# Kernel optimization log

Hardware: AMD Instinct MI355X
Metric: run time of the kernel (lower is better)

Reference implementation:

```python
import jax, jax.numpy as jnp
import numpy as np

IN_CHS = 512
RED_CHS = int(IN_CHS * 0.25)  # 128
NUM_ACTIONS = 2
BATCH = 131072


def setup_inputs() -> dict:
    key = jax.random.key(0)
    kx, k1, k2 = jax.random.split(key, 3)
    x = jax.random.normal(kx, (BATCH, IN_CHS), dtype=jnp.float32)
    # conv_reduce: Linear(in_chs, reduced_chs), conv_expand: Linear(reduced_chs, 2)
    W1 = jax.random.normal(k1, (IN_CHS, RED_CHS), dtype=jnp.float32) * 0.02
    b1 = jnp.zeros((RED_CHS,), dtype=jnp.float32)
    W2 = jax.random.normal(k2, (RED_CHS, NUM_ACTIONS), dtype=jnp.float32) * 0.02
    b2 = jnp.zeros((NUM_ACTIONS,), dtype=jnp.float32)
    return {"x": x, "W1": W1, "b1": b1, "W2": W2, "b2": b2}


def reference(x, W1, b1, W2, b2):
    # tiny 2-layer MLP head
    h = jax.nn.relu(x @ W1 + b1)                 # [B, 128]
    logits = h @ W2 + b2                         # [B, 2]
    logp = jax.nn.log_softmax(logits, axis=1)    # softmax(dim=1) in log space
    # per-row categorical sampling (np.random.choice(p=attn[id])) via Gumbel-max,
    # fused instead of a Python loop with host sync
    skey = jax.random.fold_in(jax.random.key(0), 12345)
    g = jax.random.gumbel(skey, logp.shape, dtype=logp.dtype)
    actions = jnp.argmax(logp + g, axis=1).astype(jnp.int32)  # [B]
    return actions
```

## Files before the change

### kernel.cpp

```cpp
#include <hip/hip_runtime.h>
#include <stdint.h>
#include <math.h>


#define BM 128
#define BK 32
#define LDK 40
#define IN_CHS 512
#define RED_CHS 128
#define BATCH 131072

typedef __attribute__((ext_vector_type(8))) short bf16x8;
typedef __attribute__((ext_vector_type(4))) float f32x4;

__host__ __device__ inline void tf2x32(uint32_t k0, uint32_t k1,
                                       uint32_t x0, uint32_t x1,
                                       uint32_t* o0, uint32_t* o1) {
  uint32_t ks2 = k0 ^ k1 ^ 0x1BD11BDAu;
  x0 += k0; x1 += k1;
#define TFR(r) { x0 += x1; x1 = (x1 << r) | (x1 >> (32 - r)); x1 ^= x0; }
  TFR(13) TFR(15) TFR(26) TFR(6)
  x0 += k1; x1 += ks2 + 1u;
  TFR(17) TFR(29) TFR(16) TFR(24)
  x0 += ks2; x1 += k0 + 2u;
  TFR(13) TFR(15) TFR(26) TFR(6)
  x0 += k0; x1 += k1 + 3u;
  TFR(17) TFR(29) TFR(16) TFR(24)
  x0 += k1; x1 += ks2 + 4u;
  TFR(13) TFR(15) TFR(26) TFR(6)
  x0 += ks2; x1 += k0 + 5u;
#undef TFR
  *o0 = x0; *o1 = x1;
}

__device__ __forceinline__ float gumbel_from_bits(uint32_t bits) {
  uint32_t fb = (bits >> 9) | 0x3f800000u;
  float u = __uint_as_float(fb) - 1.0f;
  if (u == 0.0f) u = 1.175494350822287508e-38f;
  float t = -(float)log((double)u);
  return -(float)log((double)t);
}

__device__ __forceinline__ unsigned short f2bf(float f) {
  uint32_t u = __float_as_uint(f);
  return (unsigned short)((u + 0x7fffu + ((u >> 16) & 1u)) >> 16);
}
__device__ __forceinline__ float bf2f(unsigned short h) {
  return __uint_as_float(((uint32_t)h) << 16);
}

__global__ __launch_bounds__(256) void rl_head_mfma(
    const float* __restrict__ x, const float* __restrict__ W1,
    const float* __restrict__ b1, const float* __restrict__ W2,
    const float* __restrict__ b2, int* __restrict__ out,
    uint32_t fk0, uint32_t fk1) {
  __shared__ __align__(16) char smem[4 * BM * LDK * 2];
  unsigned short* Ah = (unsigned short*)smem;
  unsigned short* Al = Ah + BM * LDK;
  unsigned short* Bh = Al + BM * LDK;
  float* red = (float*)smem;

  const int tid = threadIdx.x;
  const int lane = tid & 63;
  const int w = tid >> 6;
  const int ln = lane & 15;
  const int quad = lane >> 4;
  const int row0 = blockIdx.x * BM;

  const int ar = tid >> 3;
  const int ak = (tid & 7) * 4;
  const int bc = tid & 127;
  const int bk0 = (tid >> 7) * 16;

  f32x4 acc[2][8];
#pragma unroll
  for (int i = 0; i < 2; ++i)
#pragma unroll
    for (int j = 0; j < 8; ++j) acc[i][j] = (f32x4)(0.0f);

  for (int kb = 0; kb < IN_CHS; kb += BK) {
    float4 av[4];
#pragma unroll
    for (int q = 0; q < 4; ++q)
      av[q] = *(const float4*)(&x[(size_t)(row0 + q * 32 + ar) * IN_CHS + kb + ak]);
    float bv[16];
#pragma unroll
    for (int i = 0; i < 16; ++i)
      bv[i] = W1[(size_t)(kb + bk0 + i) * RED_CHS + bc];

#pragma unroll
    for (int q = 0; q < 4; ++q) {
      const int r = q * 32 + ar;
      float f[4] = {av[q].x, av[q].y, av[q].z, av[q].w};
      ushort4 h4, l4;
      unsigned short* hp = (unsigned short*)&h4;
      unsigned short* lp = (unsigned short*)&l4;
#pragma unroll
      for (int c = 0; c < 4; ++c) {
        unsigned short h = f2bf(f[c]);
        hp[c] = h;
        lp[c] = f2bf(f[c] - bf2f(h));
      }
      *(ushort4*)(&Ah[r * LDK + ak]) = h4;
      *(ushort4*)(&Al[r * LDK + ak]) = l4;
    }
    {
      ushort4 h4[4], l4[4];
#pragma unroll
      for (int g = 0; g < 4; ++g) {
        unsigned short* hp = (unsigned short*)&h4[g];
        unsigned short* lp = (unsigned short*)&l4[g];
#pragma unroll
        for (int c = 0; c < 4; ++c) {
          float f = bv[g * 4 + c];
          unsigned short h = f2bf(f);
          hp[c] = h;
          lp[c] = f2bf(f - bf2f(h));
        }
      }
#pragma unroll
      for (int g = 0; g < 4; ++g) {
        *(ushort4*)(&Bh[bc * LDK + bk0 + g * 4]) = h4[g];
        *(ushort4*)(&Bh[BM * LDK + bc * LDK + bk0 + g * 4]) = l4[g];
      }
    }
    __syncthreads();

    const unsigned short* ap = &Ah[(w * 32 + ln) * LDK + quad * 8];
    bf16x8 ah0 = *(const bf16x8*)ap;
    bf16x8 ah1 = *(const bf16x8*)(ap + 16 * LDK);
    bf16x8 al0 = *(const bf16x8*)(ap + BM * LDK);
    bf16x8 al1 = *(const bf16x8*)(ap + BM * LDK + 16 * LDK);
#pragma unroll
    for (int ct = 0; ct < 8; ++ct) {
      const unsigned short* bp = &Bh[(ct * 16 + ln) * LDK + quad * 8];
      bf16x8 bh = *(const bf16x8*)bp;
      bf16x8 bl = *(const bf16x8*)(bp + BM * LDK);
      acc[0][ct] = __builtin_amdgcn_mfma_f32_16x16x32_bf16(ah0, bh, acc[0][ct], 0, 0, 0);
      acc[0][ct] = __builtin_amdgcn_mfma_f32_16x16x32_bf16(ah0, bl, acc[0][ct], 0, 0, 0);
      acc[0][ct] = __builtin_amdgcn_mfma_f32_16x16x32_bf16(al0, bh, acc[0][ct], 0, 0, 0);
      acc[0][ct] = __builtin_amdgcn_mfma_f32_16x16x32_bf16(al0, bl, acc[0][ct], 0, 0, 0);
      acc[1][ct] = __builtin_amdgcn_mfma_f32_16x16x32_bf16(ah1, bh, acc[1][ct], 0, 0, 0);
      acc[1][ct] = __builtin_amdgcn_mfma_f32_16x16x32_bf16(ah1, bl, acc[1][ct], 0, 0, 0);
      acc[1][ct] = __builtin_amdgcn_mfma_f32_16x16x32_bf16(al1, bh, acc[1][ct], 0, 0, 0);
      acc[1][ct] = __builtin_amdgcn_mfma_f32_16x16x32_bf16(al1, bl, acc[1][ct], 0, 0, 0);
    }
    __syncthreads();
  }

  float part[8][2];
#pragma unroll
  for (int s = 0; s < 8; ++s) { part[s][0] = 0.0f; part[s][1] = 0.0f; }
#pragma unroll
  for (int ct = 0; ct < 8; ++ct) {
    const int col = ct * 16 + ln;
    const float bb = b1[col];
    const float w20 = W2[col * 2 + 0];
    const float w21 = W2[col * 2 + 1];
#pragma unroll
    for (int rt = 0; rt < 2; ++rt)
#pragma unroll
      for (int reg = 0; reg < 4; ++reg) {
        float h = acc[rt][ct][reg] + bb;
        h = h > 0.0f ? h : 0.0f;
        part[rt * 4 + reg][0] = fmaf(h, w20, part[rt * 4 + reg][0]);
        part[rt * 4 + reg][1] = fmaf(h, w21, part[rt * 4 + reg][1]);
      }
  }
#pragma unroll
  for (int rt = 0; rt < 2; ++rt)
#pragma unroll
    for (int reg = 0; reg < 4; ++reg) {
      const int row = w * 32 + rt * 16 + quad * 4 + reg;
      red[(row * 2 + 0) * 17 + ln] = part[rt * 4 + reg][0];
      red[(row * 2 + 1) * 17 + ln] = part[rt * 4 + reg][1];
    }
  __syncthreads();

  if (tid < BM) {
    const int row = tid;
    float l0 = b2[0], l1 = b2[1];
#pragma unroll
    for (int c = 0; c < 16; ++c) {
      l0 += red[(row * 2 + 0) * 17 + c];
      l1 += red[(row * 2 + 1) * 17 + c];
    }
    float m = fmaxf(l0, l1);
    float s0 = l0 - m, s1 = l1 - m;
    float e0 = (float)exp((double)s0);
    float e1 = (float)exp((double)s1);
    float lse = (float)log((double)(e0 + e1));
    float lp0 = s0 - lse, lp1 = s1 - lse;
    const int gr = row0 + row;
    uint32_t a0, a1, c0, c1;
    tf2x32(fk0, fk1, 0u, (uint32_t)(2 * gr), &a0, &a1);
    tf2x32(fk0, fk1, 0u, (uint32_t)(2 * gr + 1), &c0, &c1);
    float g0 = gumbel_from_bits(a0 ^ a1);
    float g1 = gumbel_from_bits(c0 ^ c1);
    out[gr] = ((lp1 + g1) > (lp0 + g0)) ? 1 : 0;
  }
}

extern "C" void kernel_launch(void* const* d_in, const int* in_sizes, int n_in,
                              void* d_out, int out_size, void* d_ws,
                              size_t ws_size, hipStream_t stream) {
  (void)in_sizes; (void)n_in; (void)d_ws; (void)ws_size; (void)out_size;
  const float* x = (const float*)d_in[0];
  const float* W1 = (const float*)d_in[1];
  const float* b1 = (const float*)d_in[2];
  const float* W2 = (const float*)d_in[3];
  const float* b2 = (const float*)d_in[4];
  int* out = (int*)d_out;

  uint32_t fk0, fk1;
  tf2x32(0u, 0u, 0u, 12345u, &fk0, &fk1);

  dim3 grid(BATCH / BM);
  rl_head_mfma<<<grid, 256, 0, stream>>>(x, W1, b1, W2, b2, out, fk0, fk1);
}
```

Before: 370.7 us.

## Pre-split W1 to bf16 hi/lo once and stream x directly into registers

A separate small kernel converts W1 into transposed bf16 high and low parts in workspace once per call, so blocks no longer redo that split each K step. The main kernel drops shared memory staging. Each wave loads its own x rows straight into registers with non-temporal loads and double-buffers them across K steps, and reads B fragments directly from global or L2. The final row reduction uses wave shuffles instead of an LDS pass, which removes all block barriers. The trade-off is heavier repeated global B reads per wave and an extra kernel launch.

```diff
diff --git a/kernel.cpp b/kernel.cpp
--- a/kernel.cpp
+++ b/kernel.cpp
@@ -3,15 +3,13 @@
 #include <math.h>
 
 
-#define BM 128
-#define BK 32
-#define LDK 40
 #define IN_CHS 512
 #define RED_CHS 128
 #define BATCH 131072
 
 typedef __attribute__((ext_vector_type(8))) short bf16x8;
 typedef __attribute__((ext_vector_type(4))) float f32x4;
+typedef __attribute__((ext_vector_type(4))) float vf4;
 
 __host__ __device__ inline void tf2x32(uint32_t k0, uint32_t k1,
                                        uint32_t x0, uint32_t x1,
@@ -49,28 +47,37 @@
   return __uint_as_float(((uint32_t)h) << 16);
 }
 
-__global__ __launch_bounds__(256) void rl_head_mfma(
-    const float* __restrict__ x, const float* __restrict__ W1,
-    const float* __restrict__ b1, const float* __restrict__ W2,
-    const float* __restrict__ b2, int* __restrict__ out,
-    uint32_t fk0, uint32_t fk1) {
-  __shared__ __align__(16) char smem[4 * BM * LDK * 2];
-  unsigned short* Ah = (unsigned short*)smem;
-  unsigned short* Al = Ah + BM * LDK;
-  unsigned short* Bh = Al + BM * LDK;
-  float* red = (float*)smem;
-
-  const int tid = threadIdx.x;
-  const int lane = tid & 63;
-  const int w = tid >> 6;
+__global__ __launch_bounds__(256) void w1_convert(
+    const float* __restrict__ W1, unsigned short* __restrict__ Bh,
+    unsigned short* __restrict__ Bl) {
+  const int id = blockIdx.x * 256 + threadIdx.x;
+  const int c = id >> 6;
+  const int k0 = (id & 63) * 8;
+  bf16x8 hv, lv;
+#pragma unroll
+  for (int j = 0; j < 8; ++j) {
+    float f = W1[(size_t)(k0 + j) * RED_CHS + c];
+    unsigned short h = f2bf(f);
+    hv[j] = (short)h;
+    lv[j] = (short)f2bf(f - bf2f(h));
+  }
+  *(bf16x8*)(Bh + (size_t)c * IN_CHS + k0) = hv;
+  *(bf16x8*)(Bl + (size_t)c * IN_CHS + k0) = lv;
+}
+
+__global__ __launch_bounds__(256, 3) void rl_head(
+    const float* __restrict__ x, const unsigned short* __restrict__ Bhg,
+    const unsigned short* __restrict__ Blg, const float* __restrict__ b1,
+    const float* __restrict__ W2, const float* __restrict__ b2,
+    int* __restrict__ out, uint32_t fk0, uint32_t fk1) {
+  const int lane = threadIdx.x & 63;
+  const int w = threadIdx.x >> 6;
   const int ln = lane & 15;
   const int quad = lane >> 4;
-  const int row0 = blockIdx.x * BM;
-
-  const int ar = tid >> 3;
-  const int ak = (tid & 7) * 4;
-  const int bc = tid & 127;
-  const int bk0 = (tid >> 7) * 16;
+  const int row0 = blockIdx.x * 128 + w * 32;
+
+  const float* xp0 = x + (size_t)(row0 + ln) * IN_CHS + quad * 8;
+  const float* xp1 = xp0 + (size_t)16 * IN_CHS;
 
   f32x4 acc[2][8];
 #pragma unroll
@@ -78,64 +85,39 @@
 #pragma unroll
     for (int j = 0; j < 8; ++j) acc[i][j] = (f32x4)(0.0f);
 
-  for (int kb = 0; kb < IN_CHS; kb += BK) {
-    float4 av[4];
-#pragma unroll
-    for (int q = 0; q < 4; ++q)
-      av[q] = *(const float4*)(&x[(size_t)(row0 + q * 32 + ar) * IN_CHS + kb + ak]);
-    float bv[16];
-#pragma unroll
-    for (int i = 0; i < 16; ++i)
-      bv[i] = W1[(size_t)(kb + bk0 + i) * RED_CHS + bc];
-
-#pragma unroll
-    for (int q = 0; q < 4; ++q) {
-      const int r = q * 32 + ar;
-      float f[4] = {av[q].x, av[q].y, av[q].z, av[q].w};
-      ushort4 h4, l4;
-      unsigned short* hp = (unsigned short*)&h4;
-      unsigned short* lp = (unsigned short*)&l4;
-#pragma unroll
-      for (int c = 0; c < 4; ++c) {
-        unsigned short h = f2bf(f[c]);
-        hp[c] = h;
-        lp[c] = f2bf(f[c] - bf2f(h));
+  vf4 c0a = __builtin_nontemporal_load((const vf4*)(xp0));
+  vf4 c0b = __builtin_nontemporal_load((const vf4*)(xp0 + 4));
+  vf4 c1a = __builtin_nontemporal_load((const vf4*)(xp1));
+  vf4 c1b = __builtin_nontemporal_load((const vf4*)(xp1 + 4));
+
+#pragma unroll 2
+  for (int kb = 0; kb < IN_CHS; kb += 32) {
+    vf4 n0a = {}, n0b = {}, n1a = {}, n1b = {};
+    if (kb + 32 < IN_CHS) {
+      n0a = __builtin_nontemporal_load((const vf4*)(xp0 + kb + 32));
+      n0b = __builtin_nontemporal_load((const vf4*)(xp0 + kb + 36));
+      n1a = __builtin_nontemporal_load((const vf4*)(xp1 + kb + 32));
+      n1b = __builtin_nontemporal_load((const vf4*)(xp1 + kb + 36));
+    }
+    bf16x8 ah0, al0, ah1, al1;
+    {
+      float f[8] = {c0a.x, c0a.y, c0a.z, c0a.w, c0b.x, c0b.y, c0b.z, c0b.w};
+      float g[8] = {c1a.x, c1a.y, c1a.z, c1a.w, c1b.x, c1b.y, c1b.z, c1b.w};
+#pragma unroll
+      for (int j = 0; j < 8; ++j) {
+        unsigned short h = f2bf(f[j]);
+        ah0[j] = (short)h;
+        al0[j] = (short)f2bf(f[j] - bf2f(h));
+        unsigned short h2 = f2bf(g[j]);
+        ah1[j] = (short)h2;
+        al1[j] = (short)f2bf(g[j] - bf2f(h2));
       }
-      *(ushort4*)(&Ah[r * LDK + ak]) = h4;
-      *(ushort4*)(&Al[r * LDK + ak]) = l4;
-    }
-    {
-      ushort4 h4[4], l4[4];
-#pragma unroll
-      for (int g = 0; g < 4; ++g) {
-        unsigned short* hp = (unsigned short*)&h4[g];
-        unsigned short* lp = (unsigned short*)&l4[g];
-#pragma unroll
-        for (int c = 0; c < 4; ++c) {
-          float f = bv[g * 4 + c];
-          unsigned short h = f2bf(f);
-          hp[c] = h;
-          lp[c] = f2bf(f - bf2f(h));
-        }
-      }
-#pragma unroll
-      for (int g = 0; g < 4; ++g) {
-        *(ushort4*)(&Bh[bc * LDK + bk0 + g * 4]) = h4[g];
-        *(ushort4*)(&Bh[BM * LDK + bc * LDK + bk0 + g * 4]) = l4[g];
-      }
-    }
-    __syncthreads();
-
-    const unsigned short* ap = &Ah[(w * 32 + ln) * LDK + quad * 8];
-    bf16x8 ah0 = *(const bf16x8*)ap;
-    bf16x8 ah1 = *(const bf16x8*)(ap + 16 * LDK);
-    bf16x8 al0 = *(const bf16x8*)(ap + BM * LDK);
-    bf16x8 al1 = *(const bf16x8*)(ap + BM * LDK + 16 * LDK);
+    }
 #pragma unroll
     for (int ct = 0; ct < 8; ++ct) {
-      const unsigned short* bp = &Bh[(ct * 16 + ln) * LDK + quad * 8];
-      bf16x8 bh = *(const bf16x8*)bp;
-      bf16x8 bl = *(const bf16x8*)(bp + BM * LDK);
+      const size_t boff = (size_t)(ct * 16 + ln) * IN_CHS + kb + quad * 8;
+      bf16x8 bh = *(const bf16x8*)(Bhg + boff);
+      bf16x8 bl = *(const bf16x8*)(Blg + boff);
       acc[0][ct] = __builtin_amdgcn_mfma_f32_16x16x32_bf16(ah0, bh, acc[0][ct], 0, 0, 0);
       acc[0][ct] = __builtin_amdgcn_mfma_f32_16x16x32_bf16(ah0, bl, acc[0][ct], 0, 0, 0);
       acc[0][ct] = __builtin_amdgcn_mfma_f32_16x16x32_bf16(al0, bh, acc[0][ct], 0, 0, 0);
@@ -145,12 +127,12 @@
       acc[1][ct] = __builtin_amdgcn_mfma_f32_16x16x32_bf16(al1, bh, acc[1][ct], 0, 0, 0);
       acc[1][ct] = __builtin_amdgcn_mfma_f32_16x16x32_bf16(al1, bl, acc[1][ct], 0, 0, 0);
     }
-    __syncthreads();
-  }
-
-  float part[8][2];
-#pragma unroll
-  for (int s = 0; s < 8; ++s) { part[s][0] = 0.0f; part[s][1] = 0.0f; }
+    c0a = n0a; c0b = n0b; c1a = n1a; c1b = n1b;
+  }
+
+  float p[8][2];
+#pragma unroll
+  for (int s = 0; s < 8; ++s) { p[s][0] = 0.0f; p[s][1] = 0.0f; }
 #pragma unroll
   for (int ct = 0; ct < 8; ++ct) {
     const int col = ct * 16 + ln;
@@ -163,48 +145,49 @@
       for (int reg = 0; reg < 4; ++reg) {
         float h = acc[rt][ct][reg] + bb;
         h = h > 0.0f ? h : 0.0f;
-        part[rt * 4 + reg][0] = fmaf(h, w20, part[rt * 4 + reg][0]);
-        part[rt * 4 + reg][1] = fmaf(h, w21, part[rt * 4 + reg][1]);
+        p[rt * 4 + reg][0] = fmaf(h, w20, p[rt * 4 + reg][0]);
+        p[rt * 4 + reg][1] = fmaf(h, w21, p[rt * 4 + reg][1]);
       }
   }
 #pragma unroll
-  for (int rt = 0; rt < 2; ++rt)
-#pragma unroll
-    for (int reg = 0; reg < 4; ++reg) {
-      const int row = w * 32 + rt * 16 + quad * 4 + reg;
-      red[(row * 2 + 0) * 17 + ln] = part[rt * 4 + reg][0];
-      red[(row * 2 + 1) * 17 + ln] = part[rt * 4 + reg][1];
-    }
-  __syncthreads();
-
-  if (tid < BM) {
-    const int row = tid;
-    float l0 = b2[0], l1 = b2[1];
-#pragma unroll
-    for (int c = 0; c < 16; ++c) {
-      l0 += red[(row * 2 + 0) * 17 + c];
-      l1 += red[(row * 2 + 1) * 17 + c];
-    }
+  for (int s = 0; s < 8; ++s)
+#pragma unroll
+    for (int a = 0; a < 2; ++a) {
+      float v = p[s][a];
+      v += __shfl_xor(v, 1);
+      v += __shfl_xor(v, 2);
+      v += __shfl_xor(v, 4);
+      v += __shfl_xor(v, 8);
+      p[s][a] = v;
+    }
+
+  if (ln < 8) {
+    float l0 = 0.0f, l1 = 0.0f;
+#pragma unroll
+    for (int s = 0; s < 8; ++s)
+      if (ln == s) { l0 = p[s][0]; l1 = p[s][1]; }
+    l0 += b2[0];
+    l1 += b2[1];
+    const int row = row0 + (ln >> 2) * 16 + quad * 4 + (ln & 3);
     float m = fmaxf(l0, l1);
     float s0 = l0 - m, s1 = l1 - m;
     float e0 = (float)exp((double)s0);
     float e1 = (float)exp((double)s1);
     float lse = (float)log((double)(e0 + e1));
     float lp0 = s0 - lse, lp1 = s1 - lse;
-    const int gr = row0 + row;
-    uint32_t a0, a1, c0, c1;
-    tf2x32(fk0, fk1, 0u, (uint32_t)(2 * gr), &a0, &a1);
-    tf2x32(fk0, fk1, 0u, (uint32_t)(2 * gr + 1), &c0, &c1);
+    uint32_t a0, a1, g0b, g1b;
+    tf2x32(fk0, fk1, 0u, (uint32_t)(2 * row), &a0, &a1);
+    tf2x32(fk0, fk1, 0u, (uint32_t)(2 * row + 1), &g0b, &g1b);
     float g0 = gumbel_from_bits(a0 ^ a1);
-    float g1 = gumbel_from_bits(c0 ^ c1);
-    out[gr] = ((lp1 + g1) > (lp0 + g0)) ? 1 : 0;
+    float g1 = gumbel_from_bits(g0b ^ g1b);
+    out[row] = ((lp1 + g1) > (lp0 + g0)) ? 1 : 0;
   }
 }
 
 extern "C" void kernel_launch(void* const* d_in, const int* in_sizes, int n_in,
                               void* d_out, int out_size, void* d_ws,
                               size_t ws_size, hipStream_t stream) {
-  (void)in_sizes; (void)n_in; (void)d_ws; (void)ws_size; (void)out_size;
+  (void)in_sizes; (void)n_in; (void)ws_size; (void)out_size;
   const float* x = (const float*)d_in[0];
   const float* W1 = (const float*)d_in[1];
   const float* b1 = (const float*)d_in[2];
@@ -212,9 +195,13 @@
   const float* b2 = (const float*)d_in[4];
   int* out = (int*)d_out;
 
+  unsigned short* Bh = (unsigned short*)d_ws;
+  unsigned short* Bl = Bh + (size_t)RED_CHS * IN_CHS;
+
   uint32_t fk0, fk1;
   tf2x32(0u, 0u, 0u, 12345u, &fk0, &fk1);
 
-  dim3 grid(BATCH / BM);
-  rl_head_mfma<<<grid, 256, 0, stream>>>(x, W1, b1, W2, b2, out, fk0, fk1);
-}
+  w1_convert<<<dim3(32), 256, 0, stream>>>(W1, Bh, Bl);
+  rl_head<<<dim3(BATCH / 128), 256, 0, stream>>>(x, Bh, Bl, b1, W2, b2, out,
+                                                 fk0, fk1);
+}
```

Result: slower. 498.9 us (+34.6%).
